# Performance work log

Measured on AMD Instinct MI355X. Metric: run time of the kernel, lower is better.

The kernel has to match this reference:

```python
import jax, jax.numpy as jnp
import numpy as np

N_NODES = 100000
IN_DIM = 128
HID_DIM = 128
N_EDGES = 1600000


def setup_inputs() -> dict:
    key = jax.random.key(0)
    k1, k2, k3, k4 = jax.random.split(key, 4)
    x = jax.random.normal(k1, (N_NODES, IN_DIM), dtype=jnp.float32)
    edge_index = jax.random.randint(k2, (2, N_EDGES), 0, N_NODES, dtype=jnp.int64)
    # GCNConv params (PyG: Linear(in, out, bias=False) + separate bias)
    scale = 1.0 / np.sqrt(IN_DIM)
    weight = jax.random.uniform(k3, (IN_DIM, HID_DIM), jnp.float32, -scale, scale)
    bias = jax.random.uniform(k4, (HID_DIM,), jnp.float32, -scale, scale)
    return {"x": x, "edge_index": edge_index, "weight": weight, "bias": bias}


def _gcn_forward(x, edge_index, weight, bias):
    n = x.shape[0]
    h = x @ weight  # [N, H] linear transform first (PyG order)
    # add self-loops
    loops = jnp.arange(n, dtype=edge_index.dtype)
    src = jnp.concatenate([edge_index[0], loops])
    dst = jnp.concatenate([edge_index[1], loops])
    # symmetric normalization: deg computed on destination (col) per PyG gcn_norm
    ones = jnp.ones_like(dst, dtype=h.dtype)
    deg = jax.ops.segment_sum(ones, dst, num_segments=n)  # [N]
    dinv = jnp.where(deg > 0, jax.lax.rsqrt(deg), 0.0)
    norm = dinv[src] * dinv[dst]  # [E+N]
    # message passing: out[dst] += norm * h[src]
    msg = h[src] * norm[:, None]  # [E+N, H] irregular gather (memory-bound)
    out = jax.ops.segment_sum(msg, dst, num_segments=n)  # scatter-add
    return out + bias


def reference(x, edge_index, weight, bias):
    h = _gcn_forward(x, edge_index, weight, bias)
    return jax.nn.relu(h)  # encoder_type != 'gat' -> ReLU
```

## Files before the change

kernel.cpp:

```cpp
#include <hip/hip_runtime.h>
#include <hip/hip_bf16.h>

#define N_NODES 100000
#define IN_DIM 128
#define HID_DIM 128
#define N_EDGES 1600000
#define NBK 196
#define BCAP 10240
#define BK_EDGES 4096
#define NBIN 391
#define NGEMM 1563
#define LDK 136

using half8 = __attribute__((ext_vector_type(8))) _Float16;
using half4 = __attribute__((ext_vector_type(4))) _Float16;
using f32x4 = __attribute__((ext_vector_type(4))) float;

__global__ void k_prep(int* __restrict__ gcur, const float* __restrict__ w,
                       _Float16* __restrict__ wt) {
    int i = blockIdx.x * 256 + threadIdx.x;
    if (i < NBK) gcur[i] = 0;
    if (i < IN_DIM * HID_DIM) {
        int k = i >> 7, c = i & 127;
        wt[c * 128 + k] = (_Float16)w[i];
    }
}

__global__ __launch_bounds__(256) void k_fat1(const int* __restrict__ ei,
                                              const float* __restrict__ x,
                                              const _Float16* __restrict__ wt,
                                              _Float16* __restrict__ h,
                                              int* __restrict__ gcur,
                                              uint2* __restrict__ bucket) {
    __shared__ __align__(16) char smem[52224];
    const int tid = threadIdx.x;

    if (blockIdx.x < NBIN) {
        uint2* stage = (uint2*)smem;
        int* hist  = (int*)(smem + 32768);
        int* lbase = (int*)(smem + 33552);
        int* lcur  = (int*)(smem + 34336);
        int* s64   = (int*)(smem + 35120);
        for (int b = tid; b < NBK; b += 256) { hist[b] = 0; lcur[b] = 0; }
        if (tid < 64) {
            int v = ei[2 * tid + 1];
            int all0 = __all(v == 0);
            if (tid == 0) *s64 = all0;
        }
        __syncthreads();
        const int is64 = *s64;
        const int e0 = blockIdx.x * BK_EDGES;
        const int valid = min(BK_EDGES, N_EDGES - e0);

#pragma unroll
        for (int k = 0; k < 8; ++k) {
            int el = k * 512 + 2 * tid;
            if (el >= valid) break;
            int e = e0 + el;
            int s0, s1, d0, d1;
            if (is64) {
                int4 vs = reinterpret_cast<const int4*>(ei)[e >> 1];
                int4 vd = (reinterpret_cast<const int4*>(ei) + N_EDGES / 2)[e >> 1];
                s0 = vs.x; s1 = vs.z; d0 = vd.x; d1 = vd.z;
            } else {
                int2 vs = reinterpret_cast<const int2*>(ei)[e >> 1];
                int2 vd = reinterpret_cast<const int2*>(ei + N_EDGES)[e >> 1];
                s0 = vs.x; s1 = vs.y; d0 = vd.x; d1 = vd.y;
            }
            stage[el]     = make_uint2((unsigned)s0, (unsigned)d0);
            stage[el + 1] = make_uint2((unsigned)s1, (unsigned)d1);
            atomicAdd(&hist[d0 >> 9], 1);
            atomicAdd(&hist[d1 >> 9], 1);
        }
        __syncthreads();
        for (int b = tid; b < NBK; b += 256)
            if (hist[b] > 0) lbase[b] = atomicAdd(&gcur[b], hist[b]);
        __syncthreads();
        for (int i = tid; i < valid; i += 256) {
            uint2 v = stage[i];
            int b = v.y >> 9;
            int pos = lbase[b] + atomicAdd(&lcur[b], 1);
            if (pos < BCAP) bucket[(size_t)b * BCAP + pos] = v;
        }
    } else {
        _Float16* xs = (_Float16*)smem;
        _Float16* ws = (_Float16*)(smem + 17408);
        const int brow = (blockIdx.x - NBIN) * 64;
        {
            int row = tid >> 2;
            int seg = (tid & 3) * 32;
            int grow = brow + row; if (grow > N_NODES - 1) grow = N_NODES - 1;
            const float4* p = reinterpret_cast<const float4*>(&x[(size_t)grow * IN_DIM + seg]);
#pragma unroll
            for (int i = 0; i < 8; ++i) {
                float4 v = p[i];
                half4 hv = {(_Float16)v.x, (_Float16)v.y, (_Float16)v.z, (_Float16)v.w};
                *reinterpret_cast<half4*>(&xs[row * LDK + seg + i * 4]) = hv;
            }
        }
        {
            int row = tid >> 1;
            int seg = (tid & 1) * 64;
            const half8* p = reinterpret_cast<const half8*>(&wt[row * 128 + seg]);
#pragma unroll
            for (int i = 0; i < 8; ++i)
                *reinterpret_cast<half8*>(&ws[row * LDK + seg + i * 8]) = p[i];
        }
        __syncthreads();

        const int lane = tid & 63;
        const int m0   = (tid >> 6) * 16;
        const int arow = m0 + (lane & 15);
        const int kgrp = (lane >> 4) * 8;
        f32x4 acc[8] = {};
#pragma unroll
        for (int k0 = 0; k0 < 128; k0 += 32) {
            half8 a = *reinterpret_cast<const half8*>(&xs[arow * LDK + k0 + kgrp]);
#pragma unroll
            for (int nb = 0; nb < 8; ++nb) {
                half8 b = *reinterpret_cast<const half8*>(
                    &ws[(nb * 16 + (lane & 15)) * LDK + k0 + kgrp]);
                acc[nb] = __builtin_amdgcn_mfma_f32_16x16x32_f16(a, b, acc[nb], 0, 0, 0);
            }
        }
#pragma unroll
        for (int nb = 0; nb < 8; ++nb) {
#pragma unroll
            for (int r = 0; r < 4; ++r) {
                int node = brow + m0 + (lane >> 4) * 4 + r;
                int feat = nb * 16 + (lane & 15);
                if (node < N_NODES) h[(size_t)node * HID_DIM + feat] = (_Float16)acc[nb][r];
            }
        }
    }
}

__global__ __launch_bounds__(256) void k_buildB(const int* __restrict__ gcur,
                                                const uint2* __restrict__ bucket,
                                                int* __restrict__ cnt,
                                                float* __restrict__ dinv,
                                                int* __restrict__ row_start,
                                                int* __restrict__ csr_src) {
    __shared__ int sizes[NBK];
    __shared__ int ncnt[512], nloff[512], ncur[512];
    __shared__ int wtot[4];
    __shared__ int base_s;
    const int b = blockIdx.x, tid = threadIdx.x;
    for (int i = tid; i < NBK; i += 256) sizes[i] = gcur[i];
    ncnt[tid] = 0; ncnt[tid + 256] = 0; ncur[tid] = 0; ncur[tid + 256] = 0;
    __syncthreads();
    const int sz = min(sizes[b], BCAP);
    if (tid < 64) {
        int part = 0;
        for (int i = tid; i < b; i += 64) part += sizes[i];
#pragma unroll
        for (int d = 32; d; d >>= 1) part += __shfl_xor(part, d);
        if (tid == 0) base_s = part;
    }
    const int n0 = b * 512;
    const uint2* bk = bucket + (size_t)b * BCAP;
    for (int i = tid; i < sz; i += 256) atomicAdd(&ncnt[bk[i].y - n0], 1);
    __syncthreads();
    int c0 = ncnt[2 * tid], c1 = ncnt[2 * tid + 1];
    int pair = c0 + c1;
    int lane = tid & 63, wv = tid >> 6;
    int scan = pair;
#pragma unroll
    for (int d = 1; d < 64; d <<= 1) {
        int t = __shfl_up(scan, d);
        if (lane >= d) scan += t;
    }
    if (lane == 63) wtot[wv] = scan;
    int excl = scan - pair;
    __syncthreads();
#pragma unroll
    for (int i = 0; i < 4; ++i) if (i < wv) excl += wtot[i];
    nloff[2 * tid] = excl;
    nloff[2 * tid + 1] = excl + c0;
    __syncthreads();
    const int base = base_s;
    for (int i = tid; i < 512; i += 256) {
        int node = n0 + i;
        if (node < N_NODES) {
            int c = ncnt[i];
            cnt[node] = c;
            dinv[node] = rsqrtf((float)(c + 1));
            row_start[node] = base + nloff[i];
        }
    }
    for (int i = tid; i < sz; i += 256) {
        uint2 v = bk[i];
        int li = v.y - n0;
        int pos = atomicAdd(&ncur[li], 1);
        csr_src[base + nloff[li] + pos] = (int)v.x;
    }
}

#define GSTEP(J, SE, DS) {                                                   \
    int s_ = __shfl(SE, hi | (J));                                           \
    float w_ = __shfl(DS, hi | (J));                                         \
    half8 v_ = *reinterpret_cast<const half8*>(hbase + (size_t)s_ * HID_DIM);\
    acc[0] = fmaf((float)v_[0], w_, acc[0]);                                 \
    acc[1] = fmaf((float)v_[1], w_, acc[1]);                                 \
    acc[2] = fmaf((float)v_[2], w_, acc[2]);                                 \
    acc[3] = fmaf((float)v_[3], w_, acc[3]);                                 \
    acc[4] = fmaf((float)v_[4], w_, acc[4]);                                 \
    acc[5] = fmaf((float)v_[5], w_, acc[5]);                                 \
    acc[6] = fmaf((float)v_[6], w_, acc[6]);                                 \
    acc[7] = fmaf((float)v_[7], w_, acc[7]); }
#define GGRP(B, SE, DS) \
    GSTEP(B + 0, SE, DS) GSTEP(B + 1, SE, DS) GSTEP(B + 2, SE, DS) \
    GSTEP(B + 3, SE, DS) GSTEP(B + 4, SE, DS) GSTEP(B + 5, SE, DS) \
    GSTEP(B + 6, SE, DS) GSTEP(B + 7, SE, DS)

__global__ __launch_bounds__(256) void k_gather(const _Float16* __restrict__ h,
                                                const int* __restrict__ csr_src,
                                                const int* __restrict__ row_start,
                                                const int* __restrict__ cnt,
                                                const float* __restrict__ dinv,
                                                const float* __restrict__ bias,
                                                float* __restrict__ out) {
    const int lane = threadIdx.x & 63;
    const int l4   = lane & 15;
    const int hi   = lane & 48;
    const int node = blockIdx.x * 16 + (threadIdx.x >> 6) * 4 + (lane >> 4);
    const int rs = row_start[node];
    const int n  = cnt[node];
    const float di = dinv[node];
    const int tq = n + 1;
    const _Float16* hbase = h + l4 * 8;

    float acc[8] = {};

    for (int c0 = 0; c0 < tq; c0 += 32) {
        int t0 = c0 + l4, t1 = t0 + 16;
        int se0 = node, se1 = node;
        float dw0 = 0.0f, dw1 = 0.0f;
        if (t0 < n)       { se0 = csr_src[rs + t0]; dw0 = dinv[se0]; }
        else if (t0 == n)   dw0 = di;
        if (t1 < n)       { se1 = csr_src[rs + t1]; dw1 = dinv[se1]; }
        else if (t1 == n)   dw1 = di;

        GGRP(0, se0, dw0)
        if (tq <= c0 + 8) continue;
        GGRP(8, se0, dw0)
        if (tq <= c0 + 16) continue;
        GGRP(0, se1, dw1)
        if (tq <= c0 + 24) continue;
        GGRP(8, se1, dw1)
    }

    float4 bv0 = *reinterpret_cast<const float4*>(&bias[l4 * 8]);
    float4 bv1 = *reinterpret_cast<const float4*>(&bias[l4 * 8 + 4]);
    float4 o0, o1;
    o0.x = fmaxf(fmaf(di, acc[0], bv0.x), 0.0f);
    o0.y = fmaxf(fmaf(di, acc[1], bv0.y), 0.0f);
    o0.z = fmaxf(fmaf(di, acc[2], bv0.z), 0.0f);
    o0.w = fmaxf(fmaf(di, acc[3], bv0.w), 0.0f);
    o1.x = fmaxf(fmaf(di, acc[4], bv1.x), 0.0f);
    o1.y = fmaxf(fmaf(di, acc[5], bv1.y), 0.0f);
    o1.z = fmaxf(fmaf(di, acc[6], bv1.z), 0.0f);
    o1.w = fmaxf(fmaf(di, acc[7], bv1.w), 0.0f);
    *reinterpret_cast<float4*>(&out[(size_t)node * HID_DIM + l4 * 8])     = o0;
    *reinterpret_cast<float4*>(&out[(size_t)node * HID_DIM + l4 * 8 + 4]) = o1;
}

extern "C" void kernel_launch(void* const* d_in, const int* in_sizes, int n_in,
                              void* d_out, int out_size, void* d_ws, size_t ws_size,
                              hipStream_t stream) {
    const float* x    = (const float*)d_in[0];
    const int*   ei   = (const int*)d_in[1];
    const float* w    = (const float*)d_in[2];
    const float* bias = (const float*)d_in[3];
    float* out = (float*)d_out;

    char* wsb = (char*)d_ws;
    _Float16* h      = (_Float16*)(wsb);
    int*   cnt       = (int*)(wsb + 25600000);
    float* dinv      = (float*)(wsb + 26000000);
    int*   row_start = (int*)(wsb + 26400000);
    int*   csr_src   = (int*)(wsb + 26800000);
    uint2* bucket    = (uint2*)(wsb + 33200000);
    _Float16* wt     = (_Float16*)(wsb + 49256320);
    int*   gcur      = (int*)(wsb + 49289088);

    k_prep  <<<64, 256, 0, stream>>>(gcur, w, wt);
    k_fat1  <<<NBIN + NGEMM, 256, 0, stream>>>(ei, x, wt, h, gcur, bucket);
    k_buildB<<<NBK, 256, 0, stream>>>(gcur, bucket, cnt, dinv, row_start, csr_src);
    k_gather<<<N_NODES / 16, 256, 0, stream>>>(h, csr_src, row_start, cnt, dinv, bias, out);
}
```

Before: 125.8 us.

## Split GEMM blocks across binning and CSR-build kernels to overlap work

```diff
diff --git a/kernel.cpp b/kernel.cpp
--- a/kernel.cpp
+++ b/kernel.cpp
@@ -10,6 +10,8 @@
 #define BK_EDGES 4096
 #define NBIN 391
 #define NGEMM 1563
+#define G1 625
+#define G2 (NGEMM - G1)
 #define LDK 136
 
 using half8 = __attribute__((ext_vector_type(8))) _Float16;
@@ -23,6 +25,60 @@
     if (i < IN_DIM * HID_DIM) {
         int k = i >> 7, c = i & 127;
         wt[c * 128 + k] = (_Float16)w[i];
+    }
+}
+
+__device__ __forceinline__ void gemm_role(char* smem, int tid, int brow,
+                                          const float* __restrict__ x,
+                                          const _Float16* __restrict__ wt,
+                                          _Float16* __restrict__ h) {
+    _Float16* xs = (_Float16*)smem;
+    _Float16* ws = (_Float16*)(smem + 17408);
+    {
+        int row = tid >> 2;
+        int seg = (tid & 3) * 32;
+        int grow = brow + row; if (grow > N_NODES - 1) grow = N_NODES - 1;
+        const float4* p = reinterpret_cast<const float4*>(&x[(size_t)grow * IN_DIM + seg]);
+#pragma unroll
+        for (int i = 0; i < 8; ++i) {
+            float4 v = p[i];
+            half4 hv = {(_Float16)v.x, (_Float16)v.y, (_Float16)v.z, (_Float16)v.w};
+            *reinterpret_cast<half4*>(&xs[row * LDK + seg + i * 4]) = hv;
+        }
+    }
+    {
+        int row = tid >> 1;
+        int seg = (tid & 1) * 64;
+        const half8* p = reinterpret_cast<const half8*>(&wt[row * 128 + seg]);
+#pragma unroll
+        for (int i = 0; i < 8; ++i)
+            *reinterpret_cast<half8*>(&ws[row * LDK + seg + i * 8]) = p[i];
+    }
+    __syncthreads();
+
+    const int lane = tid & 63;
+    const int m0   = (tid >> 6) * 16;
+    const int arow = m0 + (lane & 15);
+    const int kgrp = (lane >> 4) * 8;
+    f32x4 acc[8] = {};
+#pragma unroll
+    for (int k0 = 0; k0 < 128; k0 += 32) {
+        half8 a = *reinterpret_cast<const half8*>(&xs[arow * LDK + k0 + kgrp]);
+#pragma unroll
+        for (int nb = 0; nb < 8; ++nb) {
+            half8 b = *reinterpret_cast<const half8*>(
+                &ws[(nb * 16 + (lane & 15)) * LDK + k0 + kgrp]);
+            acc[nb] = __builtin_amdgcn_mfma_f32_16x16x32_f16(a, b, acc[nb], 0, 0, 0);
+        }
+    }
+#pragma unroll
+    for (int nb = 0; nb < 8; ++nb) {
+#pragma unroll
+        for (int r = 0; r < 4; ++r) {
+            int node = brow + m0 + (lane >> 4) * 4 + r;
+            int feat = nb * 16 + (lane & 15);
+            if (node < N_NODES) h[(size_t)node * HID_DIM + feat] = (_Float16)acc[nb][r];
+        }
     }
 }
 
@@ -35,117 +91,81 @@
     __shared__ __align__(16) char smem[52224];
     const int tid = threadIdx.x;
 
-    if (blockIdx.x < NBIN) {
-        uint2* stage = (uint2*)smem;
-        int* hist  = (int*)(smem + 32768);
-        int* lbase = (int*)(smem + 33552);
-        int* lcur  = (int*)(smem + 34336);
-        int* s64   = (int*)(smem + 35120);
-        for (int b = tid; b < NBK; b += 256) { hist[b] = 0; lcur[b] = 0; }
-        if (tid < 64) {
-            int v = ei[2 * tid + 1];
-            int all0 = __all(v == 0);
-            if (tid == 0) *s64 = all0;
-        }
-        __syncthreads();
-        const int is64 = *s64;
-        const int e0 = blockIdx.x * BK_EDGES;
-        const int valid = min(BK_EDGES, N_EDGES - e0);
-
-#pragma unroll
-        for (int k = 0; k < 8; ++k) {
-            int el = k * 512 + 2 * tid;
-            if (el >= valid) break;
-            int e = e0 + el;
-            int s0, s1, d0, d1;
-            if (is64) {
-                int4 vs = reinterpret_cast<const int4*>(ei)[e >> 1];
-                int4 vd = (reinterpret_cast<const int4*>(ei) + N_EDGES / 2)[e >> 1];
-                s0 = vs.x; s1 = vs.z; d0 = vd.x; d1 = vd.z;
-            } else {
-                int2 vs = reinterpret_cast<const int2*>(ei)[e >> 1];
-                int2 vd = reinterpret_cast<const int2*>(ei + N_EDGES)[e >> 1];
-                s0 = vs.x; s1 = vs.y; d0 = vd.x; d1 = vd.y;
-            }
-            stage[el]     = make_uint2((unsigned)s0, (unsigned)d0);
-            stage[el + 1] = make_uint2((unsigned)s1, (unsigned)d1);
-            atomicAdd(&hist[d0 >> 9], 1);
-            atomicAdd(&hist[d1 >> 9], 1);
-        }
-        __syncthreads();
-        for (int b = tid; b < NBK; b += 256)
-            if (hist[b] > 0) lbase[b] = atomicAdd(&gcur[b], hist[b]);
-        __syncthreads();
-        for (int i = tid; i < valid; i += 256) {
-            uint2 v = stage[i];
-            int b = v.y >> 9;
-            int pos = lbase[b] + atomicAdd(&lcur[b], 1);
-            if (pos < BCAP) bucket[(size_t)b * BCAP + pos] = v;
-        }
-    } else {
-        _Float16* xs = (_Float16*)smem;
-        _Float16* ws = (_Float16*)(smem + 17408);
-        const int brow = (blockIdx.x - NBIN) * 64;
-        {
-            int row = tid >> 2;
-            int seg = (tid & 3) * 32;
-            int grow = brow + row; if (grow > N_NODES - 1) grow = N_NODES - 1;
-            const float4* p = reinterpret_cast<const float4*>(&x[(size_t)grow * IN_DIM + seg]);
-#pragma unroll
-            for (int i = 0; i < 8; ++i) {
-                float4 v = p[i];
-                half4 hv = {(_Float16)v.x, (_Float16)v.y, (_Float16)v.z, (_Float16)v.w};
-                *reinterpret_cast<half4*>(&xs[row * LDK + seg + i * 4]) = hv;
-            }
-        }
-        {
-            int row = tid >> 1;
-            int seg = (tid & 1) * 64;
-            const half8* p = reinterpret_cast<const half8*>(&wt[row * 128 + seg]);
-#pragma unroll
-            for (int i = 0; i < 8; ++i)
-                *reinterpret_cast<half8*>(&ws[row * LDK + seg + i * 8]) = p[i];
-        }
-        __syncthreads();
-
-        const int lane = tid & 63;
-        const int m0   = (tid >> 6) * 16;
-        const int arow = m0 + (lane & 15);
-        const int kgrp = (lane >> 4) * 8;
-        f32x4 acc[8] = {};
-#pragma unroll
-        for (int k0 = 0; k0 < 128; k0 += 32) {
-            half8 a = *reinterpret_cast<const half8*>(&xs[arow * LDK + k0 + kgrp]);
-#pragma unroll
-            for (int nb = 0; nb < 8; ++nb) {
-                half8 b = *reinterpret_cast<const half8*>(
-                    &ws[(nb * 16 + (lane & 15)) * LDK + k0 + kgrp]);
-                acc[nb] = __builtin_amdgcn_mfma_f32_16x16x32_f16(a, b, acc[nb], 0, 0, 0);
-            }
-        }
-#pragma unroll
-        for (int nb = 0; nb < 8; ++nb) {
-#pragma unroll
-            for (int r = 0; r < 4; ++r) {
-                int node = brow + m0 + (lane >> 4) * 4 + r;
-                int feat = nb * 16 + (lane & 15);
-                if (node < N_NODES) h[(size_t)node * HID_DIM + feat] = (_Float16)acc[nb][r];
-            }
-        }
-    }
-}
-
-__global__ __launch_bounds__(256) void k_buildB(const int* __restrict__ gcur,
-                                                const uint2* __restrict__ bucket,
-                                                int* __restrict__ cnt,
-                                                float* __restrict__ dinv,
-                                                int* __restrict__ row_start,
-                                                int* __restrict__ csr_src) {
-    __shared__ int sizes[NBK];
-    __shared__ int ncnt[512], nloff[512], ncur[512];
-    __shared__ int wtot[4];
-    __shared__ int base_s;
-    const int b = blockIdx.x, tid = threadIdx.x;
+    if (blockIdx.x >= NBIN) {
+        gemm_role(smem, tid, (blockIdx.x - NBIN) * 64, x, wt, h);
+        return;
+    }
+    uint2* stage = (uint2*)smem;
+    int* hist  = (int*)(smem + 32768);
+    int* lbase = (int*)(smem + 33552);
+    int* lcur  = (int*)(smem + 34336);
+    int* s64   = (int*)(smem + 35120);
+    for (int b = tid; b < NBK; b += 256) { hist[b] = 0; lcur[b] = 0; }
+    if (tid < 64) {
+        int v = ei[2 * tid + 1];
+        int all0 = __all(v == 0);
+        if (tid == 0) *s64 = all0;
+    }
+    __syncthreads();
+    const int is64 = *s64;
+    const int e0 = blockIdx.x * BK_EDGES;
+    const int valid = min(BK_EDGES, N_EDGES - e0);
+
+#pragma unroll
+    for (int k = 0; k < 8; ++k) {
+        int el = k * 512 + 2 * tid;
+        if (el >= valid) break;
+        int e = e0 + el;
+        int s0, s1, d0, d1;
+        if (is64) {
+            int4 vs = reinterpret_cast<const int4*>(ei)[e >> 1];
+            int4 vd = (reinterpret_cast<const int4*>(ei) + N_EDGES / 2)[e >> 1];
+            s0 = vs.x; s1 = vs.z; d0 = vd.x; d1 = vd.z;
+        } else {
+            int2 vs = reinterpret_cast<const int2*>(ei)[e >> 1];
+            int2 vd = reinterpret_cast<const int2*>(ei + N_EDGES)[e >> 1];
+            s0 = vs.x; s1 = vs.y; d0 = vd.x; d1 = vd.y;
+        }
+        stage[el]     = make_uint2((unsigned)s0, (unsigned)d0);
+        stage[el + 1] = make_uint2((unsigned)s1, (unsigned)d1);
+        atomicAdd(&hist[d0 >> 9], 1);
+        atomicAdd(&hist[d1 >> 9], 1);
+    }
+    __syncthreads();
+    for (int b = tid; b < NBK; b += 256)
+        if (hist[b] > 0) lbase[b] = atomicAdd(&gcur[b], hist[b]);
+    __syncthreads();
+    for (int i = tid; i < valid; i += 256) {
+        uint2 v = stage[i];
+        int b = v.y >> 9;
+        int pos = lbase[b] + atomicAdd(&lcur[b], 1);
+        if (pos < BCAP) bucket[(size_t)b * BCAP + pos] = v;
+    }
+}
+
+__global__ __launch_bounds__(256) void k_fat2(const int* __restrict__ gcur,
+                                              const uint2* __restrict__ bucket,
+                                              int* __restrict__ cnt,
+                                              float* __restrict__ dinv,
+                                              int* __restrict__ row_start,
+                                              int* __restrict__ csr_src,
+                                              const float* __restrict__ x,
+                                              const _Float16* __restrict__ wt,
+                                              _Float16* __restrict__ h) {
+    __shared__ __align__(16) char smem[52224];
+    const int tid = threadIdx.x;
+
+    if (blockIdx.x >= NBK) {
+        gemm_role(smem, tid, (G1 + blockIdx.x - NBK) * 64, x, wt, h);
+        return;
+    }
+    int* sizes = (int*)smem;
+    int* ncnt  = (int*)(smem + 784);
+    int* nloff = (int*)(smem + 2832);
+    int* ncur  = (int*)(smem + 4880);
+    int* wtot  = (int*)(smem + 6928);
+    int* base_p = (int*)(smem + 6944);
+    const int b = blockIdx.x;
     for (int i = tid; i < NBK; i += 256) sizes[i] = gcur[i];
     ncnt[tid] = 0; ncnt[tid + 256] = 0; ncur[tid] = 0; ncur[tid + 256] = 0;
     __syncthreads();
@@ -155,7 +175,7 @@
         for (int i = tid; i < b; i += 64) part += sizes[i];
 #pragma unroll
         for (int d = 32; d; d >>= 1) part += __shfl_xor(part, d);
-        if (tid == 0) base_s = part;
+        if (tid == 0) *base_p = part;
     }
     const int n0 = b * 512;
     const uint2* bk = bucket + (size_t)b * BCAP;
@@ -178,7 +198,7 @@
     nloff[2 * tid] = excl;
     nloff[2 * tid + 1] = excl + c0;
     __syncthreads();
-    const int base = base_s;
+    const int base = *base_p;
     for (int i = tid; i < 512; i += 256) {
         int node = n0 + i;
         if (node < N_NODES) {
@@ -285,7 +305,7 @@
     int*   gcur      = (int*)(wsb + 49289088);
 
     k_prep  <<<64, 256, 0, stream>>>(gcur, w, wt);
-    k_fat1  <<<NBIN + NGEMM, 256, 0, stream>>>(ei, x, wt, h, gcur, bucket);
-    k_buildB<<<NBK, 256, 0, stream>>>(gcur, bucket, cnt, dinv, row_start, csr_src);
+    k_fat1  <<<NBIN + G1, 256, 0, stream>>>(ei, x, wt, h, gcur, bucket);
+    k_fat2  <<<NBK + G2, 256, 0, stream>>>(gcur, bucket, cnt, dinv, row_start, csr_src, x, wt, h);
     k_gather<<<N_NODES / 16, 256, 0, stream>>>(h, csr_src, row_start, cnt, dinv, bias, out);
 }
```

Result: no change. 123.3 us (-2.0%).
